# Kernel tuning notes

Hardware: AMD Instinct MI355X
Metric: run time of the kernel (lower is better)

The kernel has to match this reference:

```python
import jax, jax.numpy as jnp
import numpy as np

B, T, H = 512, 64, 128


def setup_inputs() -> dict:
    key = jax.random.key(0)
    ks = jax.random.split(key, 20)
    rn = lambda k, s: jax.random.normal(k, s, dtype=jnp.float32) * 0.05
    return {
        "global_features": jax.random.normal(ks[0], (B, 10, 30, 30), jnp.float32),
        "units_features": jax.random.normal(ks[1], (B, T, 8), jnp.float32),
        "conv1_w": rn(ks[2], (64, 10, 8, 8)), "conv1_b": rn(ks[3], (64,)),
        "conv2_w": rn(ks[4], (128, 64, 4, 4)), "conv2_b": rn(ks[5], (128,)),
        "ffn_map_w": rn(ks[6], (512, 3200)), "ffn_map_b": rn(ks[7], (512,)),
        "gru_wih0": rn(ks[8], (3 * H, 8)), "gru_whh0": rn(ks[9], (3 * H, H)),
        "gru_bih0": rn(ks[10], (3 * H,)), "gru_bhh0": rn(ks[11], (3 * H,)),
        "gru_wih1": rn(ks[12], (3 * H, H)), "gru_whh1": rn(ks[13], (3 * H, H)),
        "gru_bih1": rn(ks[14], (3 * H,)), "gru_bhh1": rn(ks[15], (3 * H,)),
        "joiner_w": rn(ks[16], (512, 640)), "joiner_b": rn(ks[17], (512,)),
        "out_w": rn(ks[18], (12, 512)), "out_b": rn(ks[19], (12,)),
    }


def _gru_layer(xs, wih, whh, bih, bhh):
    # xs: [L, in]; PyTorch gate order r, z, n. Precompute input gates as one GEMM.
    gi = xs @ wih.T + bih  # [L, 3H]

    def step(h, gi_t):
        gh = h @ whh.T + bhh
        i_r, i_z, i_n = jnp.split(gi_t, 3)
        h_r, h_z, h_n = jnp.split(gh, 3)
        r = jax.nn.sigmoid(i_r + h_r)
        z = jax.nn.sigmoid(i_z + h_z)
        n = jnp.tanh(i_n + r * h_n)
        h_new = (1.0 - z) * n + z * h
        return h_new, h_new

    _, hs = jax.lax.scan(step, jnp.zeros((H,), xs.dtype), gi)
    return hs  # [L, H]


def reference(global_features, units_features, conv1_w, conv1_b, conv2_w, conv2_b,
              ffn_map_w, ffn_map_b, gru_wih0, gru_whh0, gru_bih0, gru_bhh0,
              gru_wih1, gru_whh1, gru_bih1, gru_bhh1, joiner_w, joiner_b,
              out_w, out_b):
    dn = ("NCHW", "OIHW", "NCHW")
    # MapEncoder
    y = jax.lax.conv_general_dilated(global_features, conv1_w, (2, 2), "VALID",
                                     dimension_numbers=dn) + conv1_b[None, :, None, None]
    y = jax.nn.relu(y)
    y = jax.lax.conv_general_dilated(y, conv2_w, (2, 2), "VALID",
                                     dimension_numbers=dn) + conv2_b[None, :, None, None]
    y = jax.nn.relu(y)
    glob = y.reshape(-1, 3200) @ ffn_map_w.T + ffn_map_b  # [B, 512]

    # UnitRNN: the torch loop feeds x[:, k, :] (seq=B, batch=1) per step while
    # carrying hn, i.e. one long sequence of length T*B in (k, batch-row) order.
    seq = jnp.transpose(units_features, (1, 0, 2)).reshape(T * B, 8)
    h1 = _gru_layer(seq, gru_wih0, gru_whh0, gru_bih0, gru_bhh0)
    h2 = _gru_layer(h1, gru_wih1, gru_whh1, gru_bih1, gru_bhh1)
    units = h2[-B:]  # pred from final k: last-layer states over the last B steps

    hidden = jnp.concatenate([glob, units], axis=1) @ joiner_w.T + joiner_b
    out = jax.nn.relu(hidden) @ out_w.T + out_b
    return out
```

## Files before the change

kernel.cpp:

```cpp
#include <hip/hip_runtime.h>
#include <hip/hip_bf16.h>
#include <hip/hip_fp16.h>


typedef _Float16 h2_t __attribute__((ext_vector_type(2)));

#if defined(__has_builtin)
#if __has_builtin(__builtin_amdgcn_fdot2)
#define HAVE_FDOT2 1
#endif
#endif

__device__ __forceinline__ h2_t f2h2bits(float x) {
  union { float f; h2_t h; } u; u.f = x; return u.h;
}

__device__ __forceinline__ float fdot2(h2_t a, h2_t b, float c) {
#ifdef HAVE_FDOT2
  return __builtin_amdgcn_fdot2(a, b, c, false);
#else
  return c + (float)a.x * (float)b.x + (float)a.y * (float)b.y;
#endif
}

__device__ __forceinline__ float sigmoidf_(float x) {
  return 1.f / (1.f + __expf(-x));
}
__device__ __forceinline__ float tanhf_(float x) {
  return 2.f / (1.f + __expf(-2.f * x)) - 1.f;
}

__global__ __launch_bounds__(256) void conv1_k(
    const float* __restrict__ in, const float* __restrict__ w,
    const float* __restrict__ bias, float* __restrict__ out) {
  int idx = blockIdx.x * 256 + threadIdx.x;
  int pos = idx % 144;
  int co  = (idx / 144) & 63;
  int b   = idx / (144 * 64);
  int oh = pos / 12, ow = pos % 12;
  const float* ip = in + (size_t)b * 9000 + (oh * 2) * 30 + ow * 2;
  const float* wp = w + co * 640;
  float acc = bias[co];
  for (int ci = 0; ci < 10; ci++) {
#pragma unroll
    for (int kh = 0; kh < 8; kh++) {
      const float* r  = ip + ci * 900 + kh * 30;
      const float* wr = wp + ci * 64 + kh * 8;
#pragma unroll
      for (int kw = 0; kw < 8; kw++) acc += r[kw] * wr[kw];
    }
  }
  out[idx] = fmaxf(acc, 0.f);
}

__global__ __launch_bounds__(256) void conv2_k(
    const float* __restrict__ in, const float* __restrict__ w,
    const float* __restrict__ bias, float* __restrict__ out) {
  int idx = blockIdx.x * 256 + threadIdx.x;
  int pos = idx % 25;
  int co  = (idx / 25) & 127;
  int b   = idx / 3200;
  int oh = pos / 5, ow = pos % 5;
  const float* ip = in + (size_t)b * 9216 + (oh * 2) * 12 + ow * 2;
  const float* wp = w + co * 1024;
  float acc = bias[co];
  for (int ci = 0; ci < 64; ci++) {
#pragma unroll
    for (int kh = 0; kh < 4; kh++) {
      const float* r  = ip + ci * 144 + kh * 12;
      const float* wr = wp + ci * 16 + kh * 4;
#pragma unroll
      for (int kw = 0; kw < 4; kw++) acc += r[kw] * wr[kw];
    }
  }
  out[idx] = fmaxf(acc, 0.f);
}

__global__ __launch_bounds__(256) void gemm_xwt(
    const float* __restrict__ X, const float* __restrict__ W,
    const float* __restrict__ bias, float* __restrict__ C,
    int M, int N, int K, int ldc, int relu) {
  __shared__ float Xs[16][68];
  __shared__ float Ws[16][68];
  int tid = threadIdx.x;
  int m0 = blockIdx.y * 64, n0 = blockIdx.x * 64;
  int lr = tid >> 2;
  int lc = (tid & 3) << 2;
  int tm = tid >> 4, tn = tid & 15;
  float acc[4][4] = {};
  for (int k0 = 0; k0 < K; k0 += 16) {
    const float4 xv = *(const float4*)(X + (size_t)(m0 + lr) * K + k0 + lc);
    const float4 wv = *(const float4*)(W + (size_t)(n0 + lr) * K + k0 + lc);
    Xs[lc + 0][lr] = xv.x; Xs[lc + 1][lr] = xv.y;
    Xs[lc + 2][lr] = xv.z; Xs[lc + 3][lr] = xv.w;
    Ws[lc + 0][lr] = wv.x; Ws[lc + 1][lr] = wv.y;
    Ws[lc + 2][lr] = wv.z; Ws[lc + 3][lr] = wv.w;
    __syncthreads();
#pragma unroll
    for (int kk = 0; kk < 16; kk++) {
      float a[4], bb[4];
#pragma unroll
      for (int i = 0; i < 4; i++) a[i] = Xs[kk][tm * 4 + i];
#pragma unroll
      for (int j = 0; j < 4; j++) bb[j] = Ws[kk][tn * 4 + j];
#pragma unroll
      for (int i = 0; i < 4; i++)
#pragma unroll
        for (int j = 0; j < 4; j++) acc[i][j] += a[i] * bb[j];
    }
    __syncthreads();
  }
#pragma unroll
  for (int i = 0; i < 4; i++) {
    int m = m0 + tm * 4 + i;
#pragma unroll
    for (int j = 0; j < 4; j++) {
      int n = n0 + tn * 4 + j;
      float v = acc[i][j] + bias[n];
      if (relu) v = fmaxf(v, 0.f);
      C[(size_t)m * ldc + n] = v;
    }
  }
}

__global__ __launch_bounds__(384) void gi0_k(
    const float* __restrict__ uf,
    const float* __restrict__ wih,
    const float* __restrict__ bih,
    float* __restrict__ gi) {
  int n = threadIdx.x;
  int s0 = blockIdx.x * 32;
  __shared__ float xs[32][8];
  if (n < 256) {
    int ss = s0 + (n >> 3);
    int k = n & 7;
    xs[n >> 3][k] = uf[(size_t)(ss & 511) * 512 + (ss >> 9) * 8 + k];
  }
  float w[8];
#pragma unroll
  for (int k = 0; k < 8; k++) w[k] = wih[n * 8 + k];
  float b = bih[n];
  __syncthreads();
#pragma unroll 4
  for (int i = 0; i < 32; i++) {
    float a = b;
#pragma unroll
    for (int k = 0; k < 8; k++) a += w[k] * xs[i][k];
    gi[(size_t)(s0 + i) * 384 + n] = a;
  }
}

#define GRU_STEP(HIN, HOUT, G0, G1, G2, SIDX)                                 \
  {                                                                           \
    const float4* hp4 = (const float4*)(&HIN[half * 64]);                     \
    float ar = br, az = bz, an = bn;                                          \
    _Pragma("unroll")                                                         \
    for (int q = 0; q < 8; q++) {                                             \
      float4 blk = hp4[q];                                                    \
      h2_t x0 = f2h2bits(blk.x), x1 = f2h2bits(blk.y);                        \
      h2_t x2 = f2h2bits(blk.z), x3 = f2h2bits(blk.w);                        \
      ar = fdot2(wr[4*q+0], x0, ar); az = fdot2(wz[4*q+0], x0, az);           \
      an = fdot2(wn[4*q+0], x0, an);                                          \
      ar = fdot2(wr[4*q+1], x1, ar); az = fdot2(wz[4*q+1], x1, az);           \
      an = fdot2(wn[4*q+1], x1, an);                                          \
      ar = fdot2(wr[4*q+2], x2, ar); az = fdot2(wz[4*q+2], x2, az);           \
      an = fdot2(wn[4*q+2], x2, an);                                          \
      ar = fdot2(wr[4*q+3], x3, ar); az = fdot2(wz[4*q+3], x3, az);           \
      an = fdot2(wn[4*q+3], x3, an);                                          \
    }                                                                         \
    ar += __shfl_xor(ar, 1); az += __shfl_xor(az, 1); an += __shfl_xor(an, 1);\
    float r = sigmoidf_((G0) + ar);                                           \
    float z = sigmoidf_((G1) + az);                                           \
    float n = tanhf_((G2) + r * an);                                          \
    float hn = (1.f - z) * n + z * hreg;                                      \
    hreg = hn;                                                                \
    HOUT[o] = (_Float16)hn;                                                   \
    if (LAYER == 0) {                                                         \
      if (half == 0) h_out[(size_t)(SIDX) * 128 + o] = hn;                    \
    } else if ((SIDX) >= S - 512) {                                           \
      if (half == 0) jx[(size_t)((SIDX) - (S - 512)) * 640 + 512 + o] = hn;   \
    }                                                                         \
  }

#define GRU_RELOAD(G0, G1, G2)                                                \
  { G0 = gp[0]; G1 = gp[128]; G2 = gp[256]; gp += 384; }

#define GRU_BARRIER()                                                         \
  __builtin_amdgcn_sched_barrier(0);                                          \
  asm volatile("s_waitcnt lgkmcnt(0)" ::: "memory");                          \
  __builtin_amdgcn_s_barrier();                                               \
  __builtin_amdgcn_sched_barrier(0);

template <int LAYER>
__global__ __launch_bounds__(256, 1) void gru_scan3(
    const float* __restrict__ gi,
    const float* __restrict__ whh,
    const float* __restrict__ bhh,
    float* __restrict__ h_out,
    float* __restrict__ jx) {
  const int S = 32768;
  const int t = threadIdx.x;
  const int o = t >> 1;
  const int half = t & 1;

  __shared__ _Float16 hbuf0[128];
  __shared__ _Float16 hbuf1[128];

  h2_t wr[32], wz[32], wn[32];
  {
    const float2* pr = (const float2*)(whh + (size_t)(o)       * 128 + half * 64);
    const float2* pz = (const float2*)(whh + (size_t)(128 + o) * 128 + half * 64);
    const float2* pn = (const float2*)(whh + (size_t)(256 + o) * 128 + half * 64);
#pragma unroll
    for (int k = 0; k < 32; k++) {
      float2 a = pr[k], b = pz[k], c = pn[k];
      h2_t va; va.x = (_Float16)a.x; va.y = (_Float16)a.y; wr[k] = va;
      h2_t vb; vb.x = (_Float16)b.x; vb.y = (_Float16)b.y; wz[k] = vb;
      h2_t vc; vc.x = (_Float16)c.x; vc.y = (_Float16)c.y; wn[k] = vc;
    }
  }
  float br = half ? 0.f : bhh[o];
  float bz = half ? 0.f : bhh[128 + o];
  float bn = half ? 0.f : bhh[256 + o];

  float hreg = 0.f;
  if (t < 128) { hbuf0[t] = (_Float16)0.f; }

  const float* gp = gi + o;
  float gA0, gA1, gA2, gB0, gB1, gB2, gC0, gC1, gC2, gD0, gD1, gD2;
  GRU_RELOAD(gA0, gA1, gA2);
  GRU_RELOAD(gB0, gB1, gB2);
  GRU_RELOAD(gC0, gC1, gC2);
  GRU_RELOAD(gD0, gD1, gD2);
  __syncthreads();

  for (int s = 0; s < S; s += 4) {
    GRU_STEP(hbuf0, hbuf1, gA0, gA1, gA2, s);
    GRU_RELOAD(gA0, gA1, gA2);
    GRU_BARRIER();
    GRU_STEP(hbuf1, hbuf0, gB0, gB1, gB2, s + 1);
    GRU_RELOAD(gB0, gB1, gB2);
    GRU_BARRIER();
    GRU_STEP(hbuf0, hbuf1, gC0, gC1, gC2, s + 2);
    GRU_RELOAD(gC0, gC1, gC2);
    GRU_BARRIER();
    GRU_STEP(hbuf1, hbuf0, gD0, gD1, gD2, s + 3);
    GRU_RELOAD(gD0, gD1, gD2);
    GRU_BARRIER();
  }
}

__global__ __launch_bounds__(64) void out_k(
    const float* __restrict__ hidden, const float* __restrict__ ow,
    const float* __restrict__ ob, float* __restrict__ out) {
  __shared__ float hrow[512];
  int b = blockIdx.x, t = threadIdx.x;
  float4* h4 = (float4*)hrow;
  const float4* src = (const float4*)(hidden + (size_t)b * 512);
  h4[t] = src[t];
  h4[t + 64] = src[t + 64];
  __syncthreads();
  if (t < 12) {
    float acc = ob[t];
    const float* wr = ow + t * 512;
    for (int k = 0; k < 512; k++) acc += hrow[k] * wr[k];
    out[(size_t)b * 12 + t] = acc;
  }
}

extern "C" void kernel_launch(void* const* d_in, const int* in_sizes, int n_in,
                              void* d_out, int out_size, void* d_ws,
                              size_t ws_size, hipStream_t stream) {
  const float* gf    = (const float*)d_in[0];
  const float* uf    = (const float*)d_in[1];
  const float* c1w   = (const float*)d_in[2];
  const float* c1b   = (const float*)d_in[3];
  const float* c2w   = (const float*)d_in[4];
  const float* c2b   = (const float*)d_in[5];
  const float* ffw   = (const float*)d_in[6];
  const float* ffb   = (const float*)d_in[7];
  const float* wih0  = (const float*)d_in[8];
  const float* whh0  = (const float*)d_in[9];
  const float* bih0  = (const float*)d_in[10];
  const float* bhh0  = (const float*)d_in[11];
  const float* wih1  = (const float*)d_in[12];
  const float* whh1  = (const float*)d_in[13];
  const float* bih1  = (const float*)d_in[14];
  const float* bhh1  = (const float*)d_in[15];
  const float* jw    = (const float*)d_in[16];
  const float* jb    = (const float*)d_in[17];
  const float* ow    = (const float*)d_in[18];
  const float* ob    = (const float*)d_in[19];
  float* outp = (float*)d_out;

  float* ws     = (float*)d_ws;
  float* gi     = ws;
  float* conv1o = ws;
  float* conv2o = ws + 4718592;
  float* h1     = ws + 12582912;
  float* jx     = h1 + 4194304;
  float* hidden = jx + 327680;

  conv1_k<<<18432, 256, 0, stream>>>(gf, c1w, c1b, conv1o);
  conv2_k<<<6400, 256, 0, stream>>>(conv1o, c2w, c2b, conv2o);
  gemm_xwt<<<dim3(8, 8), 256, 0, stream>>>(conv2o, ffw, ffb, jx,
                                           512, 512, 3200, 640, 0);
  gi0_k<<<1024, 384, 0, stream>>>(uf, wih0, bih0, gi);
  gru_scan3<0><<<1, 256, 0, stream>>>(gi, whh0, bhh0, h1, nullptr);
  gemm_xwt<<<dim3(6, 512), 256, 0, stream>>>(h1, wih1, bih1, gi,
                                             32768, 384, 128, 384, 0);
  gru_scan3<1><<<1, 256, 0, stream>>>(gi, whh1, bhh1, nullptr, jx);
  gemm_xwt<<<dim3(8, 8), 256, 0, stream>>>(jx, jw, jb, hidden,
                                           512, 512, 640, 512, 1);
  out_k<<<512, 64, 0, stream>>>(hidden, ow, ob, outp);
}
```

Baseline: 34.04 ms.

## Split GRU recurrent dot products across four lanes per output with 512 threads

```diff
diff --git a/kernel.cpp b/kernel.cpp
--- a/kernel.cpp
+++ b/kernel.cpp
@@ -150,40 +150,43 @@
   }
 }
 
-#define GRU_STEP(HIN, HOUT, G0, G1, G2, SIDX)                                 \
+#define QSTEP(HIN, HOUT, G0, G1, G2, SIDX)                                    \
   {                                                                           \
-    const float4* hp4 = (const float4*)(&HIN[half * 64]);                     \
-    float ar = br, az = bz, an = bn;                                          \
+    const float4* hp4 = (const float4*)(&HIN[c * 32]);                        \
+    float ar = b0, az = b1, an = b2;                                          \
     _Pragma("unroll")                                                         \
-    for (int q = 0; q < 8; q++) {                                             \
+    for (int q = 0; q < 4; q++) {                                             \
       float4 blk = hp4[q];                                                    \
       h2_t x0 = f2h2bits(blk.x), x1 = f2h2bits(blk.y);                        \
       h2_t x2 = f2h2bits(blk.z), x3 = f2h2bits(blk.w);                        \
-      ar = fdot2(wr[4*q+0], x0, ar); az = fdot2(wz[4*q+0], x0, az);           \
-      an = fdot2(wn[4*q+0], x0, an);                                          \
-      ar = fdot2(wr[4*q+1], x1, ar); az = fdot2(wz[4*q+1], x1, az);           \
-      an = fdot2(wn[4*q+1], x1, an);                                          \
-      ar = fdot2(wr[4*q+2], x2, ar); az = fdot2(wz[4*q+2], x2, az);           \
-      an = fdot2(wn[4*q+2], x2, an);                                          \
-      ar = fdot2(wr[4*q+3], x3, ar); az = fdot2(wz[4*q+3], x3, az);           \
-      an = fdot2(wn[4*q+3], x3, an);                                          \
+      ar = fdot2(w0[4*q+0], x0, ar); az = fdot2(w1[4*q+0], x0, az);           \
+      an = fdot2(w2[4*q+0], x0, an);                                          \
+      ar = fdot2(w0[4*q+1], x1, ar); az = fdot2(w1[4*q+1], x1, az);           \
+      an = fdot2(w2[4*q+1], x1, an);                                          \
+      ar = fdot2(w0[4*q+2], x2, ar); az = fdot2(w1[4*q+2], x2, az);           \
+      an = fdot2(w2[4*q+2], x2, an);                                          \
+      ar = fdot2(w0[4*q+3], x3, ar); az = fdot2(w1[4*q+3], x3, az);           \
+      an = fdot2(w2[4*q+3], x3, an);                                          \
     }                                                                         \
     ar += __shfl_xor(ar, 1); az += __shfl_xor(az, 1); an += __shfl_xor(an, 1);\
+    ar += __shfl_xor(ar, 2); az += __shfl_xor(az, 2); an += __shfl_xor(an, 2);\
     float r = sigmoidf_((G0) + ar);                                           \
     float z = sigmoidf_((G1) + az);                                           \
     float n = tanhf_((G2) + r * an);                                          \
     float hn = (1.f - z) * n + z * hreg;                                      \
     hreg = hn;                                                                \
-    HOUT[o] = (_Float16)hn;                                                   \
-    if (LAYER == 0) {                                                         \
-      if (half == 0) h_out[(size_t)(SIDX) * 128 + o] = hn;                    \
-    } else if ((SIDX) >= S - 512) {                                           \
-      if (half == 0) jx[(size_t)((SIDX) - (S - 512)) * 640 + 512 + o] = hn;   \
+    if (c == 0) {                                                             \
+      HOUT[o] = (_Float16)hn;                                                 \
+      if (LAYER == 0) {                                                       \
+        h_out[(size_t)(SIDX) * 128 + o] = hn;                                 \
+      } else if ((SIDX) >= S - 512) {                                         \
+        jx[(size_t)((SIDX) - (S - 512)) * 640 + 512 + o] = hn;                \
+      }                                                                       \
     }                                                                         \
   }
 
 #define GRU_RELOAD(G0, G1, G2)                                                \
-  { G0 = gp[0]; G1 = gp[128]; G2 = gp[256]; gp += 384; }
+  { G0 = gp[0]; G1 = gp[128]; G2 = gp[256]; gp += 768; }
 
 #define GRU_BARRIER()                                                         \
   __builtin_amdgcn_sched_barrier(0);                                          \
@@ -192,7 +195,7 @@
   __builtin_amdgcn_sched_barrier(0);
 
 template <int LAYER>
-__global__ __launch_bounds__(256, 1) void gru_scan3(
+__global__ __launch_bounds__(512, 2) void gru_scan4(
     const float* __restrict__ gi,
     const float* __restrict__ whh,
     const float* __restrict__ bhh,
@@ -200,52 +203,43 @@
     float* __restrict__ jx) {
   const int S = 32768;
   const int t = threadIdx.x;
-  const int o = t >> 1;
-  const int half = t & 1;
-
-  __shared__ _Float16 hbuf0[128];
-  __shared__ _Float16 hbuf1[128];
-
-  h2_t wr[32], wz[32], wn[32];
+  const int o = t >> 2;
+  const int c = t & 3;
+
+  alignas(16) __shared__ _Float16 hbuf0[128];
+  alignas(16) __shared__ _Float16 hbuf1[128];
+
+  h2_t w0[16], w1[16], w2[16];
   {
-    const float2* pr = (const float2*)(whh + (size_t)(o)       * 128 + half * 64);
-    const float2* pz = (const float2*)(whh + (size_t)(128 + o) * 128 + half * 64);
-    const float2* pn = (const float2*)(whh + (size_t)(256 + o) * 128 + half * 64);
-#pragma unroll
-    for (int k = 0; k < 32; k++) {
-      float2 a = pr[k], b = pz[k], c = pn[k];
-      h2_t va; va.x = (_Float16)a.x; va.y = (_Float16)a.y; wr[k] = va;
-      h2_t vb; vb.x = (_Float16)b.x; vb.y = (_Float16)b.y; wz[k] = vb;
-      h2_t vc; vc.x = (_Float16)c.x; vc.y = (_Float16)c.y; wn[k] = vc;
-    }
-  }
-  float br = half ? 0.f : bhh[o];
-  float bz = half ? 0.f : bhh[128 + o];
-  float bn = half ? 0.f : bhh[256 + o];
+    const float2* pr = (const float2*)(whh + (size_t)(o)       * 128 + c * 32);
+    const float2* pz = (const float2*)(whh + (size_t)(128 + o) * 128 + c * 32);
+    const float2* pn = (const float2*)(whh + (size_t)(256 + o) * 128 + c * 32);
+#pragma unroll
+    for (int k = 0; k < 16; k++) {
+      float2 a = pr[k], b = pz[k], d = pn[k];
+      h2_t va; va.x = (_Float16)a.x; va.y = (_Float16)a.y; w0[k] = va;
+      h2_t vb; vb.x = (_Float16)b.x; vb.y = (_Float16)b.y; w1[k] = vb;
+      h2_t vc; vc.x = (_Float16)d.x; vc.y = (_Float16)d.y; w2[k] = vc;
+    }
+  }
+  float b0 = 0.f, b1 = 0.f, b2 = 0.f;
+  if (c == 0) { b0 = bhh[o]; b1 = bhh[128 + o]; b2 = bhh[256 + o]; }
 
   float hreg = 0.f;
-  if (t < 128) { hbuf0[t] = (_Float16)0.f; }
+  if (t < 128) hbuf0[t] = (_Float16)0.f;
 
   const float* gp = gi + o;
-  float gA0, gA1, gA2, gB0, gB1, gB2, gC0, gC1, gC2, gD0, gD1, gD2;
-  GRU_RELOAD(gA0, gA1, gA2);
-  GRU_RELOAD(gB0, gB1, gB2);
-  GRU_RELOAD(gC0, gC1, gC2);
-  GRU_RELOAD(gD0, gD1, gD2);
+  float gA0, gA1, gA2, gB0, gB1, gB2;
+  { gA0 = gp[0]; gA1 = gp[128]; gA2 = gp[256]; gp += 384; }
+  { gB0 = gp[0]; gB1 = gp[128]; gB2 = gp[256]; gp += 384; }
   __syncthreads();
 
-  for (int s = 0; s < S; s += 4) {
-    GRU_STEP(hbuf0, hbuf1, gA0, gA1, gA2, s);
+  for (int s = 0; s < S; s += 2) {
+    QSTEP(hbuf0, hbuf1, gA0, gA1, gA2, s);
     GRU_RELOAD(gA0, gA1, gA2);
     GRU_BARRIER();
-    GRU_STEP(hbuf1, hbuf0, gB0, gB1, gB2, s + 1);
-    GRU_RELOAD(gB0, gB1, gB2);
-    GRU_BARRIER();
-    GRU_STEP(hbuf0, hbuf1, gC0, gC1, gC2, s + 2);
-    GRU_RELOAD(gC0, gC1, gC2);
-    GRU_BARRIER();
-    GRU_STEP(hbuf1, hbuf0, gD0, gD1, gD2, s + 3);
-    GRU_RELOAD(gD0, gD1, gD2);
+    QSTEP(hbuf1, hbuf0, gB0, gB1, gB2, s + 1);
+    { gB0 = gp[-384]; gB1 = gp[-256]; gB2 = gp[-128]; }
     GRU_BARRIER();
   }
 }
@@ -306,10 +300,10 @@
   gemm_xwt<<<dim3(8, 8), 256, 0, stream>>>(conv2o, ffw, ffb, jx,
                                            512, 512, 3200, 640, 0);
   gi0_k<<<1024, 384, 0, stream>>>(uf, wih0, bih0, gi);
-  gru_scan3<0><<<1, 256, 0, stream>>>(gi, whh0, bhh0, h1, nullptr);
+  gru_scan4<0><<<1, 512, 0, stream>>>(gi, whh0, bhh0, h1, nullptr);
   gemm_xwt<<<dim3(6, 512), 256, 0, stream>>>(h1, wih1, bih1, gi,
                                              32768, 384, 128, 384, 0);
-  gru_scan3<1><<<1, 256, 0, stream>>>(gi, whh1, bhh1, nullptr, jx);
+  gru_scan4<1><<<1, 512, 0, stream>>>(gi, whh1, bhh1, nullptr, jx);
   gemm_xwt<<<dim3(8, 8), 256, 0, stream>>>(jx, jw, jb, hidden,
                                            512, 512, 640, 512, 1);
   out_k<<<512, 64, 0, stream>>>(hidden, ow, ob, outp);
```

New measurement: 39.27 ms. 1.15x slower.
